# Kernel tuning notes

Hardware: AMD Instinct MI355X
Metric: run time of the kernel (lower is better)

## Reference

```python
import jax, jax.numpy as jnp
import numpy as np


def setup_inputs() -> dict:
    key = jax.random.key(0)
    k1, k2, k3, k4 = jax.random.split(key, 4)
    Na, Nb, Da, Db, S = 200000, 200000, 64, 64, 256
    a_locations = jax.random.randint(k1, (Na, 3), 0, S, dtype=jnp.int32)
    b_locations = jax.random.randint(k2, (Nb, 3), 0, S, dtype=jnp.int32)
    a_features = jax.random.normal(k3, (Na, Da), dtype=jnp.float32)
    b_features = jax.random.normal(k4, (Nb, Db), dtype=jnp.float32)
    return {
        "a_locations": a_locations,
        "a_features": a_features,
        "b_locations": b_locations,
        "b_features": b_features,
    }


def reference(a_locations, a_features, b_locations, b_features):
    # Stack all locations and dedup rows (torch.unique(dim=0, return_inverse=True)).
    # For jit-compatibility we use size=N (worst case: no duplicates) and pad
    # trailing unused rows with fill_value=-1 (features rows stay zero).
    locations = jnp.concatenate([a_locations, b_locations], axis=0)  # [N, 3]
    N = locations.shape[0]
    unique_locations, reverse_indices = jnp.unique(
        locations, axis=0, size=N, fill_value=-1, return_inverse=True
    )
    reverse_indices = reverse_indices.ravel()  # [N]

    Na, Da = a_features.shape
    Db = b_features.shape[1]
    a_rev = reverse_indices[:Na]
    b_rev = reverse_indices[Na:]

    # Scatter-concat: a goes into columns [:Da], b into columns [Da:].
    unique_features = jnp.zeros((N, Da + Db), dtype=a_features.dtype)
    unique_features = unique_features.at[a_rev, :Da].set(a_features)
    unique_features = unique_features.at[b_rev, Da:].set(b_features)
    return unique_locations, unique_features
```

## Files before the change

### kernel.cpp

```cpp
#include <hip/hip_runtime.h>
#include <hip/hip_bf16.h>

#define NKEYS   (1 << 24)
#define NW      (NKEYS / 32)
#define TPB     256
#define NBLK    512
#define MAXN    400000

typedef float        f32x4 __attribute__((ext_vector_type(4)));
typedef unsigned int u32x4 __attribute__((ext_vector_type(4)));
typedef int          i32x4 __attribute__((ext_vector_type(4)));

__device__ unsigned int g_bits[NW];
__device__ unsigned int g_wordPrefix[NW];
__device__ unsigned int g_blockSums[NBLK];
__device__ unsigned int g_doneCounter;
__device__ int          g_winner_a[MAXN];
__device__ int          g_winner_b[MAXN];
__device__ __attribute__((aligned(16))) float g_zero[16];

__global__ void k_init() {
    int i = blockIdx.x * blockDim.x + threadIdx.x;
    reinterpret_cast<u32x4*>(g_bits)[i] = (u32x4)(0u);
    if (i == 0) g_doneCounter = 0u;
}

__global__ void k_mark4(const int* __restrict__ a_loc, const int* __restrict__ b_loc,
                        int nA4, int n4) {
    int j = blockIdx.x * blockDim.x + threadIdx.x;
    if (j >= n4) return;
    const uint4* src = (j < nA4) ? reinterpret_cast<const uint4*>(a_loc)
                                 : reinterpret_cast<const uint4*>(b_loc);
    int jj = (j < nA4) ? j : j - nA4;
    uint4 q0 = src[jj * 3], q1 = src[jj * 3 + 1], q2 = src[jj * 3 + 2];
    int k0 = (q0.x << 16) | (q0.y << 8) | q0.z;
    int k1 = (q0.w << 16) | (q1.x << 8) | q1.y;
    int k2 = (q1.z << 16) | (q1.w << 8) | q2.x;
    int k3 = (q2.y << 16) | (q2.z << 8) | q2.w;
    atomicOr(&g_bits[k0 >> 5], 1u << (k0 & 31));
    atomicOr(&g_bits[k1 >> 5], 1u << (k1 & 31));
    atomicOr(&g_bits[k2 >> 5], 1u << (k2 & 31));
    atomicOr(&g_bits[k3 >> 5], 1u << (k3 & 31));
}

__global__ void k_reduce_scan() {
    __shared__ unsigned int s[TPB];
    __shared__ unsigned int isLast;
    int b = blockIdx.x, t = threadIdx.x;
    u32x4 w = reinterpret_cast<const u32x4*>(g_bits)[b * TPB + t];
    s[t] = __popc(w.x) + __popc(w.y) + __popc(w.z) + __popc(w.w);
    __syncthreads();
    for (int off = TPB / 2; off > 0; off >>= 1) {
        if (t < off) s[t] += s[t + off];
        __syncthreads();
    }
    if (t == 0) {
        g_blockSums[b] = s[0];
        __threadfence();
        unsigned int done = atomicAdd(&g_doneCounter, 1u);
        isLast = (done == NBLK - 1) ? 1u : 0u;
    }
    __syncthreads();
    if (isLast) {
        __threadfence();
        unsigned int v0 = g_blockSums[t * 2], v1 = g_blockSums[t * 2 + 1];
        unsigned int pair = v0 + v1;
        s[t] = pair;
        __syncthreads();
        for (int off = 1; off < TPB; off <<= 1) {
            unsigned int u = (t >= off) ? s[t - off] : 0u;
            __syncthreads();
            s[t] += u;
            __syncthreads();
        }
        unsigned int excl = s[t] - pair;
        g_blockSums[t * 2]     = excl;
        g_blockSums[t * 2 + 1] = excl + v0;
    }
}

__global__ void k_prefix_loc(float* __restrict__ out_loc, int N) {
    __shared__ unsigned int s[TPB];
    __shared__ unsigned int sU;
    int b = blockIdx.x, t = threadIdx.x;

    int wi = b * TPB + t;
    if (wi < MAXN / 4) {
        reinterpret_cast<i32x4*>(g_winner_a)[wi] = (i32x4)(-1);
        reinterpret_cast<i32x4*>(g_winner_b)[wi] = (i32x4)(-1);
    }

    int w0 = (b * TPB + t) * 4;
    u32x4 wv = reinterpret_cast<const u32x4*>(g_bits)[b * TPB + t];
    unsigned int wlocal[4] = { wv.x, wv.y, wv.z, wv.w };
    unsigned int cnt = __popc(wv.x) + __popc(wv.y) + __popc(wv.z) + __popc(wv.w);
    s[t] = cnt;
    __syncthreads();
    for (int off = 1; off < TPB; off <<= 1) {
        unsigned int u = (t >= off) ? s[t - off] : 0u;
        __syncthreads();
        s[t] += u;
        __syncthreads();
    }
    unsigned int r = g_blockSums[b] + s[t] - cnt;
#pragma unroll
    for (int j = 0; j < 4; ++j) {
        unsigned int bits = wlocal[j];
        g_wordPrefix[w0 + j] = r;
        while (bits) {
            int bit = __ffs(bits) - 1;
            bits &= bits - 1;
            int key = ((w0 + j) << 5) | bit;
            float* p = out_loc + (size_t)r * 3;
            p[0] = (float)(key >> 16);
            p[1] = (float)((key >> 8) & 255);
            p[2] = (float)(key & 255);
            ++r;
        }
    }

    if (b == NBLK - 1) {
        if (t == TPB - 1) sU = r;
        __syncthreads();
        unsigned int U = sU;
        for (int i = U * 3 + t; i < N * 3; i += TPB) out_loc[i] = -1.0f;
    }
}

__global__ void k_reverse4(const int* __restrict__ a_loc, const int* __restrict__ b_loc,
                           int nA4, int n4) {
    int j = blockIdx.x * blockDim.x + threadIdx.x;
    if (j >= n4) return;
    bool isA = (j < nA4);
    const uint4* src = isA ? reinterpret_cast<const uint4*>(a_loc)
                           : reinterpret_cast<const uint4*>(b_loc);
    int jj = isA ? j : j - nA4;
    uint4 q0 = src[jj * 3], q1 = src[jj * 3 + 1], q2 = src[jj * 3 + 2];
    int key[4];
    key[0] = (q0.x << 16) | (q0.y << 8) | q0.z;
    key[1] = (q0.w << 16) | (q1.x << 8) | q1.y;
    key[2] = (q1.z << 16) | (q1.w << 8) | q2.x;
    key[3] = (q2.y << 16) | (q2.z << 8) | q2.w;
    int* winner = isA ? g_winner_a : g_winner_b;
    int base = jj * 4;
#pragma unroll
    for (int k = 0; k < 4; ++k) {
        int kk = key[k];
        unsigned int word = g_bits[kk >> 5];
        unsigned int r = g_wordPrefix[kk >> 5] + __popc(word & ((1u << (kk & 31)) - 1u));
        atomicMax(&winner[r], base + k);
    }
}

__global__ void k_mark1(const int* __restrict__ a_loc, const int* __restrict__ b_loc,
                        int Na, int N) {
    int i = blockIdx.x * blockDim.x + threadIdx.x;
    if (i >= N) return;
    const int* p = (i < Na) ? (a_loc + (size_t)i * 3) : (b_loc + (size_t)(i - Na) * 3);
    int key = (p[0] << 16) | (p[1] << 8) | p[2];
    atomicOr(&g_bits[key >> 5], 1u << (key & 31));
}
__global__ void k_reverse1(const int* __restrict__ a_loc, const int* __restrict__ b_loc,
                           int Na, int N) {
    int i = blockIdx.x * blockDim.x + threadIdx.x;
    if (i >= N) return;
    const int* p = (i < Na) ? (a_loc + (size_t)i * 3) : (b_loc + (size_t)(i - Na) * 3);
    int key = (p[0] << 16) | (p[1] << 8) | p[2];
    unsigned int word = g_bits[key >> 5];
    unsigned int r = g_wordPrefix[key >> 5] + __popc(word & ((1u << (key & 31)) - 1u));
    if (i < Na) atomicMax(&g_winner_a[r], i);
    else        atomicMax(&g_winner_b[r], i - Na);
}

__global__ void k_gather(const float* __restrict__ a_feat, const float* __restrict__ b_feat,
                         float* __restrict__ out_feat, int N) {
    int idx = blockIdx.x * blockDim.x + threadIdx.x;
    if (idx >= N * 8) return;
    int u    = idx >> 3;
    int c    = idx & 7;
    bool isB = (c >= 4);
    int col  = (c & 3) * 16;

    const int* wtab = isB ? g_winner_b : g_winner_a;
    int w = wtab[u];

    const float* fbase = isB ? b_feat : a_feat;
    const float* src = (w >= 0) ? (fbase + (size_t)w * 64 + col) : g_zero;

    f32x4 v0 = *reinterpret_cast<const f32x4*>(src);
    f32x4 v1 = *reinterpret_cast<const f32x4*>(src + 4);
    f32x4 v2 = *reinterpret_cast<const f32x4*>(src + 8);
    f32x4 v3 = *reinterpret_cast<const f32x4*>(src + 12);

    float* dst = out_feat + (size_t)u * 128 + c * 16;
    *reinterpret_cast<f32x4*>(dst)      = v0;
    *reinterpret_cast<f32x4*>(dst + 4)  = v1;
    *reinterpret_cast<f32x4*>(dst + 8)  = v2;
    *reinterpret_cast<f32x4*>(dst + 12) = v3;
}

extern "C" void kernel_launch(void* const* d_in, const int* in_sizes, int n_in,
                              void* d_out, int out_size, void* d_ws, size_t ws_size,
                              hipStream_t stream) {
    const int*   a_loc  = (const int*)  d_in[0];
    const float* a_feat = (const float*)d_in[1];
    const int*   b_loc  = (const int*)  d_in[2];
    const float* b_feat = (const float*)d_in[3];

    const int Na = in_sizes[0] / 3;
    const int Nb = in_sizes[2] / 3;
    const int N  = Na + Nb;

    float* out_loc  = (float*)d_out;
    float* out_feat = out_loc + (size_t)N * 3;

    k_init<<<NW / 4 / TPB, TPB, 0, stream>>>();

    if ((Na % 4) == 0 && (Nb % 4) == 0) {
        int nA4 = Na / 4, n4 = (Na + Nb) / 4;
        k_mark4<<<(n4 + TPB - 1) / TPB, TPB, 0, stream>>>(a_loc, b_loc, nA4, n4);
        k_reduce_scan<<<NBLK, TPB, 0, stream>>>();
        k_prefix_loc<<<NBLK, TPB, 0, stream>>>(out_loc, N);
        k_reverse4<<<(n4 + TPB - 1) / TPB, TPB, 0, stream>>>(a_loc, b_loc, nA4, n4);
    } else {
        k_mark1<<<(N + TPB - 1) / TPB, TPB, 0, stream>>>(a_loc, b_loc, Na, N);
        k_reduce_scan<<<NBLK, TPB, 0, stream>>>();
        k_prefix_loc<<<NBLK, TPB, 0, stream>>>(out_loc, N);
        k_reverse1<<<(N + TPB - 1) / TPB, TPB, 0, stream>>>(a_loc, b_loc, Na, N);
    }

    k_gather<<<(N * 8 + TPB - 1) / TPB, TPB, 0, stream>>>(a_feat, b_feat, out_feat, N);
}
```

Baseline: 156.0 us.

## Replace winner-indexed gather with per-input rank scatter plus zero-fill

The reverse pass now stores each input row's unique rank in a new g_rank array. The final gather kernel is replaced by one launch that splits into two block ranges. One range zero-fills output half-rows that have no winner. The other has each winning input row copy its features into its rank's slot. Reads of feature rows become sequential in input order instead of random by winner index, while output writes become scattered, and g_rank adds extra traffic plus an extra winner lookup per input row.

New measurement: 152.5 us (median of 2 runs). 1.02x faster.

```diff
diff --git a/kernel.cpp b/kernel.cpp
--- a/kernel.cpp
+++ b/kernel.cpp
@@ -17,7 +17,7 @@
 __device__ unsigned int g_doneCounter;
 __device__ int          g_winner_a[MAXN];
 __device__ int          g_winner_b[MAXN];
-__device__ __attribute__((aligned(16))) float g_zero[16];
+__device__ unsigned int g_rank[MAXN];
 
 __global__ void k_init() {
     int i = blockIdx.x * blockDim.x + threadIdx.x;
@@ -57,8 +57,7 @@
     if (t == 0) {
         g_blockSums[b] = s[0];
         __threadfence();
-        unsigned int done = atomicAdd(&g_doneCounter, 1u);
-        isLast = (done == NBLK - 1) ? 1u : 0u;
+        isLast = (atomicAdd(&g_doneCounter, 1u) == NBLK - 1) ? 1u : 0u;
     }
     __syncthreads();
     if (isLast) {
@@ -83,15 +82,13 @@
     __shared__ unsigned int s[TPB];
     __shared__ unsigned int sU;
     int b = blockIdx.x, t = threadIdx.x;
-
     int wi = b * TPB + t;
     if (wi < MAXN / 4) {
         reinterpret_cast<i32x4*>(g_winner_a)[wi] = (i32x4)(-1);
         reinterpret_cast<i32x4*>(g_winner_b)[wi] = (i32x4)(-1);
     }
-
-    int w0 = (b * TPB + t) * 4;
-    u32x4 wv = reinterpret_cast<const u32x4*>(g_bits)[b * TPB + t];
+    int w0 = wi * 4;
+    u32x4 wv = reinterpret_cast<const u32x4*>(g_bits)[wi];
     unsigned int wlocal[4] = { wv.x, wv.y, wv.z, wv.w };
     unsigned int cnt = __popc(wv.x) + __popc(wv.y) + __popc(wv.z) + __popc(wv.w);
     s[t] = cnt;
@@ -108,27 +105,22 @@
         unsigned int bits = wlocal[j];
         g_wordPrefix[w0 + j] = r;
         while (bits) {
-            int bit = __ffs(bits) - 1;
-            bits &= bits - 1;
+            int bit = __ffs(bits) - 1; bits &= bits - 1;
             int key = ((w0 + j) << 5) | bit;
             float* p = out_loc + (size_t)r * 3;
-            p[0] = (float)(key >> 16);
-            p[1] = (float)((key >> 8) & 255);
-            p[2] = (float)(key & 255);
+            p[0] = (float)(key >> 16); p[1] = (float)((key >> 8) & 255); p[2] = (float)(key & 255);
             ++r;
         }
     }
-
     if (b == NBLK - 1) {
         if (t == TPB - 1) sU = r;
         __syncthreads();
-        unsigned int U = sU;
-        for (int i = U * 3 + t; i < N * 3; i += TPB) out_loc[i] = -1.0f;
+        for (int i = (int)sU * 3 + t; i < N * 3; i += TPB) out_loc[i] = -1.0f;
     }
 }
 
 __global__ void k_reverse4(const int* __restrict__ a_loc, const int* __restrict__ b_loc,
-                           int nA4, int n4) {
+                           int nA4, int n4, int Na) {
     int j = blockIdx.x * blockDim.x + threadIdx.x;
     if (j >= n4) return;
     bool isA = (j < nA4);
@@ -143,13 +135,17 @@
     key[3] = (q2.y << 16) | (q2.z << 8) | q2.w;
     int* winner = isA ? g_winner_a : g_winner_b;
     int base = jj * 4;
+    int gbase = isA ? base : (Na + base);
+    u32x4 rv;
 #pragma unroll
     for (int k = 0; k < 4; ++k) {
         int kk = key[k];
         unsigned int word = g_bits[kk >> 5];
         unsigned int r = g_wordPrefix[kk >> 5] + __popc(word & ((1u << (kk & 31)) - 1u));
         atomicMax(&winner[r], base + k);
-    }
+        ((unsigned int*)&rv)[k] = r;
+    }
+    reinterpret_cast<u32x4*>(g_rank)[gbase >> 2] = rv;
 }
 
 __global__ void k_mark1(const int* __restrict__ a_loc, const int* __restrict__ b_loc,
@@ -170,33 +166,48 @@
     unsigned int r = g_wordPrefix[key >> 5] + __popc(word & ((1u << (key & 31)) - 1u));
     if (i < Na) atomicMax(&g_winner_a[r], i);
     else        atomicMax(&g_winner_b[r], i - Na);
-}
-
-__global__ void k_gather(const float* __restrict__ a_feat, const float* __restrict__ b_feat,
-                         float* __restrict__ out_feat, int N) {
-    int idx = blockIdx.x * blockDim.x + threadIdx.x;
-    if (idx >= N * 8) return;
-    int u    = idx >> 3;
-    int c    = idx & 7;
-    bool isB = (c >= 4);
-    int col  = (c & 3) * 16;
-
-    const int* wtab = isB ? g_winner_b : g_winner_a;
-    int w = wtab[u];
-
-    const float* fbase = isB ? b_feat : a_feat;
-    const float* src = (w >= 0) ? (fbase + (size_t)w * 64 + col) : g_zero;
-
-    f32x4 v0 = *reinterpret_cast<const f32x4*>(src);
-    f32x4 v1 = *reinterpret_cast<const f32x4*>(src + 4);
-    f32x4 v2 = *reinterpret_cast<const f32x4*>(src + 8);
-    f32x4 v3 = *reinterpret_cast<const f32x4*>(src + 12);
-
-    float* dst = out_feat + (size_t)u * 128 + c * 16;
-    *reinterpret_cast<f32x4*>(dst)      = v0;
-    *reinterpret_cast<f32x4*>(dst + 4)  = v1;
-    *reinterpret_cast<f32x4*>(dst + 8)  = v2;
-    *reinterpret_cast<f32x4*>(dst + 12) = v3;
+    g_rank[i] = r;
+}
+
+__global__ void k_zero_scatter(const float* __restrict__ a_feat, const float* __restrict__ b_feat,
+                               float* __restrict__ out_feat, int Na, int N, int zblk) {
+    int b = blockIdx.x, t = threadIdx.x;
+    if (b < zblk) {
+        int idx = b * TPB + t;
+        if (idx >= N * 8) return;
+        int u = idx >> 3;
+        int h = (idx >> 2) & 1;
+        int c = idx & 3;
+        int w = h ? g_winner_b[u] : g_winner_a[u];
+        if (w < 0) {
+            float* dst = out_feat + (size_t)u * 128 + h * 64 + c * 16;
+            f32x4 z = (f32x4)(0.f);
+            *reinterpret_cast<f32x4*>(dst)      = z;
+            *reinterpret_cast<f32x4*>(dst + 4)  = z;
+            *reinterpret_cast<f32x4*>(dst + 8)  = z;
+            *reinterpret_cast<f32x4*>(dst + 12) = z;
+        }
+    } else {
+        int idx = (b - zblk) * TPB + t;
+        if (idx >= N * 4) return;
+        int i = idx >> 2;
+        int c = idx & 3;
+        bool isA = (i < Na);
+        int ii = isA ? i : i - Na;
+        unsigned int r = g_rank[i];
+        int w = isA ? g_winner_a[r] : g_winner_b[r];
+        if (w != ii) return;
+        const float* src = (isA ? a_feat : b_feat) + (size_t)ii * 64 + c * 16;
+        f32x4 v0 = *reinterpret_cast<const f32x4*>(src);
+        f32x4 v1 = *reinterpret_cast<const f32x4*>(src + 4);
+        f32x4 v2 = *reinterpret_cast<const f32x4*>(src + 8);
+        f32x4 v3 = *reinterpret_cast<const f32x4*>(src + 12);
+        float* dst = out_feat + (size_t)r * 128 + (isA ? 0 : 64) + c * 16;
+        *reinterpret_cast<f32x4*>(dst)      = v0;
+        *reinterpret_cast<f32x4*>(dst + 4)  = v1;
+        *reinterpret_cast<f32x4*>(dst + 8)  = v2;
+        *reinterpret_cast<f32x4*>(dst + 12) = v3;
+    }
 }
 
 extern "C" void kernel_launch(void* const* d_in, const int* in_sizes, int n_in,
@@ -221,7 +232,7 @@
         k_mark4<<<(n4 + TPB - 1) / TPB, TPB, 0, stream>>>(a_loc, b_loc, nA4, n4);
         k_reduce_scan<<<NBLK, TPB, 0, stream>>>();
         k_prefix_loc<<<NBLK, TPB, 0, stream>>>(out_loc, N);
-        k_reverse4<<<(n4 + TPB - 1) / TPB, TPB, 0, stream>>>(a_loc, b_loc, nA4, n4);
+        k_reverse4<<<(n4 + TPB - 1) / TPB, TPB, 0, stream>>>(a_loc, b_loc, nA4, n4, Na);
     } else {
         k_mark1<<<(N + TPB - 1) / TPB, TPB, 0, stream>>>(a_loc, b_loc, Na, N);
         k_reduce_scan<<<NBLK, TPB, 0, stream>>>();
@@ -229,5 +240,7 @@
         k_reverse1<<<(N + TPB - 1) / TPB, TPB, 0, stream>>>(a_loc, b_loc, Na, N);
     }
 
-    k_gather<<<(N * 8 + TPB - 1) / TPB, TPB, 0, stream>>>(a_feat, b_feat, out_feat, N);
-}
+    int zblk = (N * 8 + TPB - 1) / TPB;
+    int sblk = (N * 4 + TPB - 1) / TPB;
+    k_zero_scatter<<<zblk + sblk, TPB, 0, stream>>>(a_feat, b_feat, out_feat, Na, N, zblk);
+}
```
